# Kernel tuning notes

Hardware: AMD Instinct MI355X
Metric: run time of the kernel (lower is better)

Reference implementation:

```python
import jax, jax.numpy as jnp
import numpy as np

N_ENT, N_CON, DIM, R, NB = 30000, 29309, 128, 12, 8
B, LC, S, E_DB, E_CON = 256, 50, 32, 300000, 200000


def setup_inputs() -> dict:
    key = jax.random.key(0)
    ks = jax.random.split(key, 32)
    f = lambda k, sh: (jax.random.normal(k, sh, jnp.float32) * 0.02)
    concept_emb = f(ks[0], (N_CON, DIM)).at[0].set(0.0)  # padding_idx=0 row zeroed
    inp = {
        'concept_mask': jax.random.randint(ks[1], (B, LC), 0, N_CON, jnp.int32),
        'seed_pad': jax.random.randint(ks[2], (B, S), 0, N_ENT, jnp.int32),
        'seed_lens': jax.random.randint(ks[3], (B,), 0, S + 1, jnp.int32),
        'db_edge_index': jax.random.randint(ks[4], (2, E_DB), 0, N_ENT, jnp.int32),
        'db_edge_type': jax.random.randint(ks[5], (E_DB,), 0, R, jnp.int32),
        'con_edge_index': jax.random.randint(ks[6], (2, E_CON), 0, N_CON, jnp.int32),
        'db_vec': jax.random.uniform(ks[7], (B, N_ENT), jnp.float32),
        'labels': jax.random.randint(ks[8], (B,), 0, N_ENT, jnp.int64),
        'rec': jax.random.uniform(ks[9], (B,), jnp.float32),
        'concept_emb': concept_emb,
        'basis': f(ks[10], (NB, N_ENT, DIM)),
        'comp': f(ks[11], (R, NB)),
        'rgcn_root': f(ks[12], (N_ENT, DIM)),
        'rgcn_bias': jnp.zeros((DIM,), jnp.float32),
        'gcn_w': f(ks[13], (DIM, DIM)),
        'gcn_b': jnp.zeros((DIM,), jnp.float32),
        'attn_a': f(ks[14], (DIM, DIM)),
        'attn_b': f(ks[15], (DIM, 1)),
        'attn_a_db': f(ks[16], (DIM, DIM)),
        'attn_b_db': f(ks[17], (DIM, 1)),
        'user_norm_w': f(ks[18], (DIM, 2 * DIM)),
        'user_norm_b': jnp.zeros((DIM,), jnp.float32),
        'gate_norm_w': f(ks[19], (1, DIM)),
        'gate_norm_b': jnp.zeros((1,), jnp.float32),
        'info_con_w': f(ks[20], (DIM, DIM)),
        'info_con_b': jnp.zeros((DIM,), jnp.float32),
        'info_out_db_b': jnp.zeros((N_ENT,), jnp.float32),
        'output_en_b': jnp.zeros((N_ENT,), jnp.float32),
    }
    return inp


def _forward(concept_mask, seed_pad, seed_lens, db_edge_index, db_edge_type,
             con_edge_index, db_vec, labels, rec, concept_emb, basis, comp,
             rgcn_root, rgcn_bias, gcn_w, gcn_b, attn_a, attn_b, attn_a_db,
             attn_b_db, user_norm_w, user_norm_b, gate_norm_w, gate_norm_b,
             info_con_w, info_con_b, info_out_db_b, output_en_b):
    NEG = jnp.float32(-1e30)
    # ---- RGCN over DBpedia graph (x=None -> per-edge row W[rel][src]) ----
    w = jnp.einsum('rb,bnd->rnd', comp, basis)            # [R, N_ent, D]
    src, dst = db_edge_index[0], db_edge_index[1]
    msg = w[db_edge_type, src]                            # [E, D]
    agg = jax.ops.segment_sum(msg, dst, num_segments=N_ENT)
    cnt = jax.ops.segment_sum(jnp.ones_like(dst, jnp.float32), dst, num_segments=N_ENT)
    db_feats = agg / jnp.maximum(cnt, 1.0)[:, None] + rgcn_root + rgcn_bias  # mean aggr + root + bias
    # ---- GCN over concept graph (symmetric norm, self-loops) ----
    xw = concept_emb @ gcn_w
    loops = jnp.arange(N_CON, dtype=con_edge_index.dtype)
    cs = jnp.concatenate([con_edge_index[0], loops])
    cd = jnp.concatenate([con_edge_index[1], loops])
    deg = jax.ops.segment_sum(jnp.ones_like(cd, jnp.float32), cd, num_segments=N_CON)
    dinv = jnp.where(deg > 0, jax.lax.rsqrt(jnp.maximum(deg, 1e-12)), 0.0)
    norm = dinv[cs] * dinv[cd]
    con_feats = jax.ops.segment_sum(norm[:, None] * xw[cs], cd, num_segments=N_CON) + gcn_b
    # ---- per-sample seed-set self-attention over db features ----
    h = db_feats[seed_pad]                                # [B, S, D]
    e = jnp.tanh(h @ attn_a_db) @ attn_b_db               # [B, S, 1]
    valid = jnp.arange(S)[None, :] < seed_lens[:, None]   # [B, S]
    a = jax.nn.softmax(jnp.where(valid[..., None], e, NEG), axis=1)
    db_user = jnp.einsum('bso,bsd->bd', a, h)             # weighted sum (o=1)
    has_seed = (seed_lens > 0)
    db_user = jnp.where(has_seed[:, None], db_user, 0.0)  # empty seed set -> zeros
    db_con_mask = has_seed.astype(jnp.float32)
    # ---- batch self-attention over gathered concept features ----
    hc = con_feats[concept_mask]                          # [B, LC, D]
    ec = jnp.tanh(hc @ attn_a) @ attn_b                   # [B, LC, 1]
    cvalid = (concept_mask != 0)
    ac = jax.nn.softmax(jnp.where(cvalid[..., None], ec, NEG), axis=1)
    con_user = jnp.einsum('blo,bld->bd', ac, hc)
    # ---- gated fusion ----
    u = jnp.concatenate([con_user, db_user], axis=-1) @ user_norm_w.T + user_norm_b
    gate = jax.nn.sigmoid(u @ gate_norm_w.T + gate_norm_b)  # [B, 1]
    user_emb = gate * db_user + (1.0 - gate) * con_user
    entity_scores = user_emb @ db_feats.T + output_en_b   # [B, N_ent]
    # ---- infomax MSE loss ----
    con_e = con_user @ info_con_w.T + info_con_b
    db_scores = con_e @ db_feats.T + info_out_db_b
    info_db_loss = jnp.mean(jnp.sum((db_scores - db_vec) ** 2, axis=-1) * db_con_mask)
    # ---- rec CE loss ----
    logp = jax.nn.log_softmax(entity_scores, axis=-1)
    ce = -jnp.take_along_axis(logp, labels[:, None].astype(jnp.int32), axis=1)[:, 0]
    rec_loss = jnp.sum(ce * rec)
    loss = rec_loss + 0.025 * info_db_loss                # pretrain=False path
    return loss, entity_scores, rec_loss


def reference(concept_mask, seed_pad, seed_lens, db_edge_index, db_edge_type,
              con_edge_index, db_vec, labels, rec, concept_emb, basis, comp,
              rgcn_root, rgcn_bias, gcn_w, gcn_b, attn_a, attn_b, attn_a_db,
              attn_b_db, user_norm_w, user_norm_b, gate_norm_w, gate_norm_b,
              info_con_w, info_con_b, info_out_db_b, output_en_b):
    return _forward(concept_mask, seed_pad, seed_lens, db_edge_index, db_edge_type,
                    con_edge_index, db_vec, labels, rec, concept_emb, basis, comp,
                    rgcn_root, rgcn_bias, gcn_w, gcn_b, attn_a, attn_b, attn_a_db,
                    attn_b_db, user_norm_w, user_norm_b, gate_norm_w, gate_norm_b,
                    info_con_w, info_con_b, info_out_db_b, output_en_b)
```

## Files before the change

kernel.cpp:

```cpp
#include <hip/hip_runtime.h>

#define N_ENT  30000
#define N_CON  29309
#define DIM    128
#define NBASIS 8
#define NREL   12
#define BATCH  256
#define LCON   50
#define SSEED  32
#define EDB    300000
#define ECON   200000
#define NTILE  938

#define NE4      ((N_CON * DIM) / 4)
#define NB_HIST  ((EDB + ECON + 255) / 256)
#define NB_CONV  ((NE4 + 3 * (DIM * DIM / 4) + 255) / 256)
#define NB_WCOMP ((N_ENT * 32) / 256)
#define NB_XW    ((N_CON + 127) / 128)
#define NB_RG    ((N_ENT + 3) / 4)
#define NB_GG    ((N_CON + 3) / 4)
#define NB_EDB   ((N_ENT + 31) / 32)
#define NB_ECON  ((N_CON + 31) / 32)

typedef __attribute__((ext_vector_type(8)))  short bfrag8;
typedef __attribute__((ext_vector_type(16))) float facc16;

__device__ __forceinline__ unsigned short f2bf(float f) {
    unsigned int u = __float_as_uint(f);
    u += 0x7FFFu + ((u >> 16) & 1u);
    return (unsigned short)(u >> 16);
}
__device__ __forceinline__ float bf2f(unsigned int h) {
    return __uint_as_float(h << 16);
}

__global__ __launch_bounds__(256) void prep_kernel(const int* __restrict__ db_dst,
                                                   const int* __restrict__ con_dst,
                                                   const float* __restrict__ emb,
                                                   const float* __restrict__ W,
                                                   const float* __restrict__ A_db,
                                                   const float* __restrict__ A_c,
                                                   const float* __restrict__ basis,
                                                   const float* __restrict__ comp,
                                                   int* __restrict__ cnt_e, int* __restrict__ cnt_c,
                                                   int* __restrict__ ord_db, int* __restrict__ ord_con,
                                                   unsigned short* __restrict__ emb_h,
                                                   unsigned short* __restrict__ Wt_h,
                                                   unsigned short* __restrict__ At_db_h,
                                                   unsigned short* __restrict__ At_c_h,
                                                   unsigned short* __restrict__ w_h,
                                                   int use_w) {
    __shared__ float sc[NREL * NBASIS];
    int t = threadIdx.x, bb = blockIdx.x;
    if (bb < NB_HIST) {
        int e = bb * 256 + t;
        if (e < EDB) {
            ord_db[e] = atomicAdd(cnt_e + db_dst[e], 1);
        } else if (e < EDB + ECON) {
            int ee = e - EDB;
            ord_con[ee] = atomicAdd(cnt_c + con_dst[ee], 1);
        }
        return;
    }
    if (bb < NB_HIST + NB_CONV) {
        int i = (bb - NB_HIST) * 256 + t;
        if (i < NE4) {
            float4 v = ((const float4*)emb)[i];
            unsigned int p0 = (unsigned int)f2bf(v.x) | ((unsigned int)f2bf(v.y) << 16);
            unsigned int p1 = (unsigned int)f2bf(v.z) | ((unsigned int)f2bf(v.w) << 16);
            *(uint2*)(emb_h + (size_t)i * 4) = make_uint2(p0, p1);
        } else {
            int j = i - NE4;
            if (j < 3 * (DIM * DIM) / 4) {
                int sel = j >> 12;
                int jj = j & 4095;
                const float* S = (sel == 0) ? W : ((sel == 1) ? A_db : A_c);
                unsigned short* Dst = (sel == 0) ? Wt_h : ((sel == 1) ? At_db_h : At_c_h);
                int o = jj * 4;
                int n = o >> 7, k0 = o & 127;
                unsigned int p0 = (unsigned int)f2bf(S[(k0 + 0) * DIM + n]) |
                                  ((unsigned int)f2bf(S[(k0 + 1) * DIM + n]) << 16);
                unsigned int p1 = (unsigned int)f2bf(S[(k0 + 2) * DIM + n]) |
                                  ((unsigned int)f2bf(S[(k0 + 3) * DIM + n]) << 16);
                *(uint2*)(Dst + n * DIM + k0) = make_uint2(p0, p1);
            }
        }
        return;
    }
    if (!use_w) return;
    if (t < NREL * NBASIS) sc[t] = comp[t];
    __syncthreads();
    int i = (bb - NB_HIST - NB_CONV) * 256 + t;
    int n = i >> 5, d4 = i & 31;
    float4 bv[NBASIS];
#pragma unroll
    for (int b = 0; b < NBASIS; ++b)
        bv[b] = ((const float4*)(basis + ((size_t)b * N_ENT + n) * DIM))[d4];
#pragma unroll
    for (int r = 0; r < NREL; ++r) {
        float4 acc = make_float4(0.f, 0.f, 0.f, 0.f);
#pragma unroll
        for (int b = 0; b < NBASIS; ++b) {
            float c = sc[r * NBASIS + b];
            acc.x += c * bv[b].x; acc.y += c * bv[b].y;
            acc.z += c * bv[b].z; acc.w += c * bv[b].w;
        }
        unsigned int p0 = (unsigned int)f2bf(acc.x) | ((unsigned int)f2bf(acc.y) << 16);
        unsigned int p1 = (unsigned int)f2bf(acc.z) | ((unsigned int)f2bf(acc.w) << 16);
        *(uint2*)(w_h + ((size_t)r * N_ENT + n) * DIM + d4 * 4) = make_uint2(p0, p1);
    }
}

__device__ void scan_block(const int* __restrict__ cnt, int n, int* __restrict__ rowptr) {
    __shared__ int part[1024];
    int t = threadIdx.x;
    int per = (n + 1023) / 1024;
    int s0 = t * per;
    int sum = 0;
    for (int i = 0; i < per; ++i) {
        int idx = s0 + i;
        if (idx < n) sum += cnt[idx];
    }
    part[t] = sum;
    __syncthreads();
    for (int off = 1; off < 1024; off <<= 1) {
        int v = (t >= off) ? part[t - off] : 0;
        __syncthreads();
        part[t] += v;
        __syncthreads();
    }
    int run = part[t] - sum;
    for (int i = 0; i < per; ++i) {
        int idx = s0 + i;
        if (idx < n) {
            rowptr[idx] = run;
            run += cnt[idx];
        }
    }
    if (t == 1023) rowptr[n] = part[1023];
}

__global__ __launch_bounds__(1024) void scan2_kernel(const int* __restrict__ cnt_e,
                                                     const int* __restrict__ cnt_c,
                                                     int* __restrict__ rowptr_e,
                                                     int* __restrict__ rowptr_c,
                                                     float* __restrict__ dinv,
                                                     const unsigned short* __restrict__ emb_h,
                                                     const unsigned short* __restrict__ Wt_h,
                                                     unsigned short* __restrict__ xw_h) {
    int bb = blockIdx.x;
    if (bb == 0) {
        scan_block(cnt_e, N_ENT, rowptr_e);
        return;
    }
    if (bb == 1) {
        scan_block(cnt_c, N_CON, rowptr_c);
        for (int i = threadIdx.x; i < N_CON; i += 1024)
            dinv[i] = rsqrtf((float)(cnt_c[i] + 1));
        return;
    }
    int t = threadIdx.x;
    int wave = t >> 6, lane = t & 63;
    int m0 = (bb - 2) * 128 + (wave >> 2) * 32;
    int n0 = (wave & 3) * 32;
    int am = lane & 31, ak = (lane >> 5) * 8;
    int mrow = m0 + am;
    bool mv = mrow < N_CON;
    const unsigned short* Ar = emb_h + (size_t)mrow * DIM + ak;
    const unsigned short* Br = Wt_h + (size_t)(n0 + am) * DIM + ak;
    facc16 acc;
#pragma unroll
    for (int r = 0; r < 16; ++r) acc[r] = 0.f;
#pragma unroll
    for (int s = 0; s < 8; ++s) {
        bfrag8 a;
#pragma unroll
        for (int j = 0; j < 8; ++j) a[j] = 0;
        if (mv) a = *(const bfrag8*)(Ar + s * 16);
        bfrag8 b = *(const bfrag8*)(Br + s * 16);
        acc = __builtin_amdgcn_mfma_f32_32x32x16_bf16(a, b, acc, 0, 0, 0);
    }
    int col = lane & 31;
    int g4 = (lane >> 5) * 4;
#pragma unroll
    for (int r = 0; r < 16; ++r) {
        int m = m0 + (r & 3) + ((r >> 2) << 3) + g4;
        if (m < N_CON) xw_h[(size_t)m * DIM + n0 + col] = f2bf(acc[r]);
    }
}

__global__ __launch_bounds__(256) void scatter_kernel(const int* __restrict__ db_eidx,
                                                      const int* __restrict__ db_etype,
                                                      const int* __restrict__ con_eidx,
                                                      const int* __restrict__ ord_db,
                                                      const int* __restrict__ ord_con,
                                                      const int* __restrict__ rowptr_e,
                                                      const int* __restrict__ rowptr_c,
                                                      int* __restrict__ elist_e,
                                                      int* __restrict__ elist_c) {
    int e = blockIdx.x * 256 + threadIdx.x;
    if (e < EDB) {
        int dst = db_eidx[EDB + e];
        elist_e[rowptr_e[dst] + ord_db[e]] = db_eidx[e] | (db_etype[e] << 18);
    } else if (e < EDB + ECON) {
        int ee = e - EDB;
        int dst = con_eidx[ECON + ee];
        elist_c[rowptr_c[dst] + ord_con[ee]] = con_eidx[ee];
    }
}

__global__ __launch_bounds__(256) void gathers_kernel(const int* __restrict__ rowptr_e,
                                                      const int* __restrict__ elist_e,
                                                      const unsigned short* __restrict__ w_h,
                                                      const float* __restrict__ root,
                                                      const float* __restrict__ bias,
                                                      unsigned short* __restrict__ dbf_h,
                                                      const int* __restrict__ rowptr_c,
                                                      const int* __restrict__ elist_c,
                                                      const float* __restrict__ dinv,
                                                      const unsigned short* __restrict__ xw_h,
                                                      const float* __restrict__ gcn_b,
                                                      unsigned short* __restrict__ conf_h) {
    int bb = blockIdx.x;
    int lane = threadIdx.x & 63;
    if (bb < NB_RG) {
        int wid = bb * 4 + (threadIdx.x >> 6);
        if (wid >= N_ENT) return;
        int beg = rowptr_e[wid], end = rowptr_e[wid + 1];
        float a0 = 0.f, a1 = 0.f;
        int p = beg;
        for (; p + 3 < end; p += 4) {
            int v0 = elist_e[p], v1 = elist_e[p + 1], v2 = elist_e[p + 2], v3 = elist_e[p + 3];
            unsigned int k0 = *(const unsigned int*)(w_h + ((size_t)(v0 >> 18) * N_ENT + (v0 & 0x3FFFF)) * DIM + lane * 2);
            unsigned int k1 = *(const unsigned int*)(w_h + ((size_t)(v1 >> 18) * N_ENT + (v1 & 0x3FFFF)) * DIM + lane * 2);
            unsigned int k2 = *(const unsigned int*)(w_h + ((size_t)(v2 >> 18) * N_ENT + (v2 & 0x3FFFF)) * DIM + lane * 2);
            unsigned int k3 = *(const unsigned int*)(w_h + ((size_t)(v3 >> 18) * N_ENT + (v3 & 0x3FFFF)) * DIM + lane * 2);
            a0 += bf2f(k0 & 0xFFFF) + bf2f(k1 & 0xFFFF) + bf2f(k2 & 0xFFFF) + bf2f(k3 & 0xFFFF);
            a1 += bf2f(k0 >> 16)    + bf2f(k1 >> 16)    + bf2f(k2 >> 16)    + bf2f(k3 >> 16);
        }
        for (; p < end; ++p) {
            int v = elist_e[p];
            unsigned int k = *(const unsigned int*)(w_h + ((size_t)(v >> 18) * N_ENT + (v & 0x3FFFF)) * DIM + lane * 2);
            a0 += bf2f(k & 0xFFFF);
            a1 += bf2f(k >> 16);
        }
        float inv = 1.f / fmaxf((float)(end - beg), 1.f);
        size_t base = (size_t)wid * DIM + lane * 2;
        float f0 = a0 * inv + root[base]     + bias[lane * 2];
        float f1 = a1 * inv + root[base + 1] + bias[lane * 2 + 1];
        *(unsigned int*)(dbf_h + base) = (unsigned int)f2bf(f0) | ((unsigned int)f2bf(f1) << 16);
    } else {
        int wid = (bb - NB_RG) * 4 + (threadIdx.x >> 6);
        if (wid >= N_CON) return;
        int beg = rowptr_c[wid], end = rowptr_c[wid + 1];
        float a0 = 0.f, a1 = 0.f;
        int p = beg;
        for (; p + 3 < end; p += 4) {
            int s0 = elist_c[p], s1 = elist_c[p + 1], s2 = elist_c[p + 2], s3 = elist_c[p + 3];
            float n0 = dinv[s0], n1 = dinv[s1], n2 = dinv[s2], n3 = dinv[s3];
            unsigned int k0 = *(const unsigned int*)(xw_h + (size_t)s0 * DIM + lane * 2);
            unsigned int k1 = *(const unsigned int*)(xw_h + (size_t)s1 * DIM + lane * 2);
            unsigned int k2 = *(const unsigned int*)(xw_h + (size_t)s2 * DIM + lane * 2);
            unsigned int k3 = *(const unsigned int*)(xw_h + (size_t)s3 * DIM + lane * 2);
            a0 += n0 * bf2f(k0 & 0xFFFF) + n1 * bf2f(k1 & 0xFFFF) + n2 * bf2f(k2 & 0xFFFF) + n3 * bf2f(k3 & 0xFFFF);
            a1 += n0 * bf2f(k0 >> 16)    + n1 * bf2f(k1 >> 16)    + n2 * bf2f(k2 >> 16)    + n3 * bf2f(k3 >> 16);
        }
        for (; p < end; ++p) {
            int s = elist_c[p];
            float nm = dinv[s];
            unsigned int k = *(const unsigned int*)(xw_h + (size_t)s * DIM + lane * 2);
            a0 += nm * bf2f(k & 0xFFFF);
            a1 += nm * bf2f(k >> 16);
        }
        float dv = dinv[wid];
        unsigned int ks = *(const unsigned int*)(xw_h + (size_t)wid * DIM + lane * 2);
        size_t base = (size_t)wid * DIM + lane * 2;
        float f0 = dv * a0 + dv * dv * bf2f(ks & 0xFFFF) + gcn_b[lane * 2];
        float f1 = dv * a1 + dv * dv * bf2f(ks >> 16)    + gcn_b[lane * 2 + 1];
        *(unsigned int*)(conf_h + base) = (unsigned int)f2bf(f0) | ((unsigned int)f2bf(f1) << 16);
    }
}

__global__ __launch_bounds__(256) void rgcn_gather_basis(const int* __restrict__ rowptr,
                                                         const int* __restrict__ elist,
                                                         const float* __restrict__ basis,
                                                         const float* __restrict__ comp,
                                                         const float* __restrict__ root,
                                                         const float* __restrict__ bias,
                                                         unsigned short* __restrict__ dbf_h) {
    int wid  = blockIdx.x * 4 + (threadIdx.x >> 6);
    int lane = threadIdx.x & 63;
    if (wid >= N_ENT) return;
    int beg = rowptr[wid], end = rowptr[wid + 1];
    float a0 = 0.f, a1 = 0.f;
    for (int p = beg; p < end; ++p) {
        int v = elist[p];
        int src = v & 0x3FFFF, ty = v >> 18;
        const float* c = comp + ty * NBASIS;
#pragma unroll
        for (int b = 0; b < NBASIS; ++b) {
            const float* bp = basis + ((size_t)b * N_ENT + src) * DIM;
            a0 += c[b] * bp[lane * 2];
            a1 += c[b] * bp[lane * 2 + 1];
        }
    }
    float inv = 1.f / fmaxf((float)(end - beg), 1.f);
    size_t base = (size_t)wid * DIM + lane * 2;
    float f0 = a0 * inv + root[base]     + bias[lane * 2];
    float f1 = a1 * inv + root[base + 1] + bias[lane * 2 + 1];
    *(unsigned int*)(dbf_h + base) = (unsigned int)f2bf(f0) | ((unsigned int)f2bf(f1) << 16);
}

__global__ __launch_bounds__(256) void escore_kernel(const unsigned short* __restrict__ dbf_h,
                                                     const unsigned short* __restrict__ conf_h,
                                                     const unsigned short* __restrict__ At_db_h,
                                                     const float* __restrict__ v_db,
                                                     const unsigned short* __restrict__ At_c_h,
                                                     const float* __restrict__ v_c,
                                                     float* __restrict__ e_db,
                                                     float* __restrict__ e_con) {
    __shared__ float part[4][32];
    int t = threadIdx.x, bb = blockIdx.x;
    int wave = t >> 6, lane = t & 63;
    const unsigned short* feats;
    const unsigned short* At;
    const float* v;
    float* eo;
    int m0, nrow;
    if (bb < NB_EDB) {
        feats = dbf_h;  At = At_db_h; v = v_db; eo = e_db;  m0 = bb * 32;             nrow = N_ENT;
    } else {
        feats = conf_h; At = At_c_h;  v = v_c;  eo = e_con; m0 = (bb - NB_EDB) * 32;  nrow = N_CON;
    }
    int n0 = wave * 32;
    int am = lane & 31, ak = (lane >> 5) * 8;
    int mrow = m0 + am;
    bool mv = mrow < nrow;
    const unsigned short* Ar = feats + (size_t)mrow * DIM + ak;
    const unsigned short* Br = At + (size_t)(n0 + am) * DIM + ak;
    facc16 acc;
#pragma unroll
    for (int r = 0; r < 16; ++r) acc[r] = 0.f;
#pragma unroll
    for (int s = 0; s < 8; ++s) {
        bfrag8 a;
#pragma unroll
        for (int j = 0; j < 8; ++j) a[j] = 0;
        if (mv) a = *(const bfrag8*)(Ar + s * 16);
        bfrag8 b = *(const bfrag8*)(Br + s * 16);
        acc = __builtin_amdgcn_mfma_f32_32x32x16_bf16(a, b, acc, 0, 0, 0);
    }
    int col = lane & 31, g = lane >> 5;
    float vn = v[n0 + col];
#pragma unroll
    for (int r = 0; r < 16; ++r) {
        float x = tanhf(acc[r]) * vn;
#pragma unroll
        for (int off = 16; off >= 1; off >>= 1) x += __shfl_xor(x, off, 32);
        if (col == 0) {
            int row = (r & 3) + ((r >> 2) << 3) + (g << 2);
            part[wave][row] = x;
        }
    }
    __syncthreads();
    if (t < 32) {
        int m = m0 + t;
        if (m < nrow)
            eo[m] = part[0][t] + part[1][t] + part[2][t] + part[3][t];
    }
}

__global__ __launch_bounds__(256) void attn_fusion_kernel(const unsigned short* __restrict__ dbf_h,
                                                          const unsigned short* __restrict__ conf_h,
                                                          const float* __restrict__ e_db,
                                                          const float* __restrict__ e_con,
                                                          const int* __restrict__ seed_pad,
                                                          const int* __restrict__ seed_lens,
                                                          const int* __restrict__ concept_mask,
                                                          const float* __restrict__ Wu, const float* __restrict__ bu,
                                                          const float* __restrict__ gw, const float* __restrict__ gb,
                                                          const float* __restrict__ Wi, const float* __restrict__ bi,
                                                          unsigned short* __restrict__ uemb_h,
                                                          unsigned short* __restrict__ cone_h,
                                                          float* __restrict__ maskv) {
    __shared__ int srow[SSEED];
    __shared__ int crow[LCON];
    __shared__ float a_db[SSEED], a_con[LCON];
    __shared__ float du[DIM], cu[DIM], red[DIM];
    int b = blockIdx.x, t = threadIdx.x;
    int wave = t >> 6, lane = t & 63;
    int len = seed_lens[b];
    if (wave == 0) {
        float e = -1e30f;
        if (lane < SSEED) {
            int rv = seed_pad[b * SSEED + lane];
            srow[lane] = rv;
            if (lane < len) e = e_db[rv];
        }
        float m = e;
#pragma unroll
        for (int off = 16; off >= 1; off >>= 1) m = fmaxf(m, __shfl_xor(m, off, 32));
        float p = (lane < SSEED) ? __expf(e - m) : 0.f;
        float s = p;
#pragma unroll
        for (int off = 16; off >= 1; off >>= 1) s += __shfl_xor(s, off, 32);
        if (lane < SSEED) a_db[lane] = p / s;
    } else if (wave == 1) {
        float e = -1e30f;
        if (lane < LCON) {
            int rv = concept_mask[b * LCON + lane];
            crow[lane] = rv;
            if (rv != 0) e = e_con[rv];
        }
        float m = e;
#pragma unroll
        for (int off = 32; off >= 1; off >>= 1) m = fmaxf(m, __shfl_xor(m, off, 64));
        float p = (lane < LCON) ? __expf(e - m) : 0.f;
        float s = p;
#pragma unroll
        for (int off = 32; off >= 1; off >>= 1) s += __shfl_xor(s, off, 64);
        if (lane < LCON) a_con[lane] = p / s;
    }
    __syncthreads();
    if (t < DIM) {
        float acc = 0.f;
#pragma unroll
        for (int s = 0; s < SSEED; ++s)
            acc += a_db[s] * bf2f((unsigned int)dbf_h[(size_t)srow[s] * DIM + t]);
        du[t] = (len > 0) ? acc : 0.f;
    } else {
        int d = t - DIM;
        float acc = 0.f;
#pragma unroll
        for (int s = 0; s < LCON; ++s)
            acc += a_con[s] * bf2f((unsigned int)conf_h[(size_t)crow[s] * DIM + d]);
        cu[d] = acc;
    }
    __syncthreads();
    if (t < DIM) {
        float u = bu[t];
        const float* wr = Wu + t * 2 * DIM;
        for (int k = 0; k < DIM; ++k) u += cu[k] * wr[k];
        for (int k = 0; k < DIM; ++k) u += du[k] * wr[DIM + k];
        red[t] = u * gw[t];
    }
    __syncthreads();
    for (int s2 = 64; s2 > 0; s2 >>= 1) {
        if (t < s2) red[t] += red[t + s2];
        __syncthreads();
    }
    if (t < DIM) {
        float gate = 1.f / (1.f + __expf(-(red[0] + gb[0])));
        uemb_h[b * DIM + t] = f2bf(gate * du[t] + (1.f - gate) * cu[t]);
        float ce = bi[t];
        const float* wi = Wi + t * DIM;
        for (int k = 0; k < DIM; ++k) ce += cu[k] * wi[k];
        cone_h[b * DIM + t] = f2bf(ce);
    }
    if (t == 0) maskv[b] = (len > 0) ? 1.f : 0.f;
}

__global__ __launch_bounds__(256) void score_mfma(const unsigned short* __restrict__ dbf_h,
                                                  const unsigned short* __restrict__ uemb_h,
                                                  const unsigned short* __restrict__ cone_h,
                                                  const float* __restrict__ en_b,
                                                  const float* __restrict__ info_b,
                                                  const float* __restrict__ db_vec,
                                                  float* __restrict__ escore,
                                                  float* __restrict__ partM,
                                                  float* __restrict__ partS,
                                                  float* __restrict__ partQ) {
    int wave = threadIdx.x >> 6, lane = threadIdx.x & 63;
    int nt = blockIdx.x * 4 + wave;
    if (nt >= NTILE) return;
    int b0 = blockIdx.y * 32;
    int n0 = nt * 32;
    int am = lane & 31, ak = (lane >> 5) * 8;
    int nb = n0 + am;
    bool bvalid = nb < N_ENT;
    const unsigned short* Au = uemb_h + (size_t)(b0 + am) * DIM + ak;
    const unsigned short* Ac = cone_h + (size_t)(b0 + am) * DIM + ak;
    const unsigned short* Bp = dbf_h + (size_t)nb * DIM + ak;
    facc16 accE, accD;
#pragma unroll
    for (int r = 0; r < 16; ++r) { accE[r] = 0.f; accD[r] = 0.f; }
#pragma unroll
    for (int s = 0; s < 8; ++s) {
        bfrag8 au = *(const bfrag8*)(Au + s * 16);
        bfrag8 ac = *(const bfrag8*)(Ac + s * 16);
        bfrag8 bb;
#pragma unroll
        for (int j = 0; j < 8; ++j) bb[j] = 0;
        if (bvalid) bb = *(const bfrag8*)(Bp + s * 16);
        accE = __builtin_amdgcn_mfma_f32_32x32x16_bf16(au, bb, accE, 0, 0, 0);
        accD = __builtin_amdgcn_mfma_f32_32x32x16_bf16(ac, bb, accD, 0, 0, 0);
    }
    int col = lane & 31;
    int n = n0 + col;
    bool nv = n < N_ENT;
    float enb = nv ? en_b[n] : 0.f;
    float inb = nv ? info_b[n] : 0.f;
    int g4 = (lane >> 5) * 4;
#pragma unroll
    for (int r = 0; r < 16; ++r) {
        int b = b0 + (r & 3) + ((r >> 2) << 3) + g4;
        float e = accE[r] + enb;
        if (nv) escore[(size_t)b * N_ENT + n] = e;
        float ev = nv ? e : -1e30f;
        float mx = ev;
#pragma unroll
        for (int off = 16; off >= 1; off >>= 1) mx = fmaxf(mx, __shfl_xor(mx, off, 64));
        float ex = nv ? __expf(e - mx) : 0.f;
        float sm = ex;
#pragma unroll
        for (int off = 16; off >= 1; off >>= 1) sm += __shfl_xor(sm, off, 64);
        float d = nv ? (accD[r] + inb - db_vec[(size_t)b * N_ENT + n]) : 0.f;
        float q = d * d;
#pragma unroll
        for (int off = 16; off >= 1; off >>= 1) q += __shfl_xor(q, off, 64);
        if (col == 0) {
            partM[(size_t)b * NTILE + nt] = mx;
            partS[(size_t)b * NTILE + nt] = sm;
            partQ[(size_t)b * NTILE + nt] = q;
        }
    }
}

__global__ __launch_bounds__(256) void ce_final(const float* __restrict__ partM,
                                                const float* __restrict__ partS,
                                                const float* __restrict__ partQ,
                                                const float* __restrict__ escore,
                                                const int* __restrict__ labels,
                                                const float* __restrict__ rec,
                                                float* __restrict__ rloss,
                                                float* __restrict__ ssqv) {
    __shared__ float red[256], red2[256];
    int b = blockIdx.x, t = threadIdx.x;
    const float* pm = partM + (size_t)b * NTILE;
    const float* ps = partS + (size_t)b * NTILE;
    const float* pq = partQ + (size_t)b * NTILE;
    float mx = -1e30f;
    for (int i = t; i < NTILE; i += 256) mx = fmaxf(mx, pm[i]);
    red[t] = mx;
    __syncthreads();
    for (int s2 = 128; s2 > 0; s2 >>= 1) {
        if (t < s2) red[t] = fmaxf(red[t], red[t + s2]);
        __syncthreads();
    }
    float M = red[0];
    __syncthreads();
    float s = 0.f, q = 0.f;
    for (int i = t; i < NTILE; i += 256) {
        s += ps[i] * __expf(pm[i] - M);
        q += pq[i];
    }
    red[t] = s; red2[t] = q;
    __syncthreads();
    for (int s2 = 128; s2 > 0; s2 >>= 1) {
        if (t < s2) { red[t] += red[t + s2]; red2[t] += red2[t + s2]; }
        __syncthreads();
    }
    if (t == 0) {
        float lse = M + logf(red[0]);
        float ce  = -(escore[(size_t)b * N_ENT + labels[b]] - lse);
        rloss[b]  = ce * rec[b];
        ssqv[b]   = red2[0];
    }
}

__global__ __launch_bounds__(256) void final_kernel(const float* __restrict__ rloss,
                                                    const float* __restrict__ sumsq,
                                                    const float* __restrict__ maskv,
                                                    float* __restrict__ out) {
    __shared__ float r1[256], r2[256];
    int t = threadIdx.x;
    r1[t] = rloss[t];
    r2[t] = sumsq[t] * maskv[t];
    __syncthreads();
    for (int s2 = 128; s2 > 0; s2 >>= 1) {
        if (t < s2) { r1[t] += r1[t + s2]; r2[t] += r2[t + s2]; }
        __syncthreads();
    }
    if (t == 0) {
        float rec_loss = r1[0];
        float info = r2[0] / (float)BATCH;
        out[0] = rec_loss + 0.025f * info;
        out[1 + (size_t)BATCH * N_ENT] = rec_loss;
    }
}

extern "C" void kernel_launch(void* const* d_in, const int* in_sizes, int n_in,
                              void* d_out, int out_size, void* d_ws, size_t ws_size,
                              hipStream_t stream) {
    (void)in_sizes; (void)n_in; (void)out_size;
    const int*   concept_mask  = (const int*)d_in[0];
    const int*   seed_pad      = (const int*)d_in[1];
    const int*   seed_lens     = (const int*)d_in[2];
    const int*   db_eidx       = (const int*)d_in[3];
    const int*   db_etype      = (const int*)d_in[4];
    const int*   con_eidx      = (const int*)d_in[5];
    const float* db_vec        = (const float*)d_in[6];
    const int*   labels        = (const int*)d_in[7];
    const float* rec           = (const float*)d_in[8];
    const float* concept_emb   = (const float*)d_in[9];
    const float* basis         = (const float*)d_in[10];
    const float* comp          = (const float*)d_in[11];
    const float* rgcn_root     = (const float*)d_in[12];
    const float* rgcn_bias     = (const float*)d_in[13];
    const float* gcn_w         = (const float*)d_in[14];
    const float* gcn_b         = (const float*)d_in[15];
    const float* attn_a        = (const float*)d_in[16];
    const float* attn_b        = (const float*)d_in[17];
    const float* attn_a_db     = (const float*)d_in[18];
    const float* attn_b_db     = (const float*)d_in[19];
    const float* user_norm_w   = (const float*)d_in[20];
    const float* user_norm_b   = (const float*)d_in[21];
    const float* gate_norm_w   = (const float*)d_in[22];
    const float* gate_norm_b   = (const float*)d_in[23];
    const float* info_con_w    = (const float*)d_in[24];
    const float* info_con_b    = (const float*)d_in[25];
    const float* info_out_db_b = (const float*)d_in[26];
    const float* output_en_b   = (const float*)d_in[27];

    float* ws = (float*)d_ws;
    size_t off = 0;
    auto alloc = [&](size_t n) { float* p = ws + off; off += (n + 255) & ~(size_t)255; return p; };
    float* dinv   = alloc(N_CON);
    float* maskv  = alloc(BATCH);
    float* rls    = alloc(BATCH);
    float* ssqv   = alloc(BATCH);
    float* partM  = alloc((size_t)BATCH * NTILE);
    float* partS  = alloc((size_t)BATCH * NTILE);
    float* partQ  = alloc((size_t)BATCH * NTILE);
    int* cnt_e    = (int*)alloc(N_ENT + N_CON);
    int* cnt_c    = cnt_e + N_ENT;
    int* rowptr_e = (int*)alloc(N_ENT + 1);
    int* rowptr_c = (int*)alloc(N_CON + 1);
    int* ord_db   = (int*)alloc(EDB);
    int* ord_con  = (int*)alloc(ECON);
    int* elist_e  = (int*)alloc(EDB);
    int* elist_c  = (int*)alloc(ECON);
    unsigned short* dbf_h  = (unsigned short*)alloc((size_t)N_ENT * DIM / 2);
    unsigned short* conf_h = (unsigned short*)alloc((size_t)N_CON * DIM / 2 + 128);
    unsigned short* xw_h   = (unsigned short*)alloc((size_t)N_CON * DIM / 2 + 128);
    unsigned short* emb_h  = (unsigned short*)alloc((size_t)N_CON * DIM / 2 + 128);
    unsigned short* Wt_h   = (unsigned short*)alloc(DIM * DIM / 2);
    unsigned short* uemb_h = (unsigned short*)alloc(BATCH * DIM / 2);
    unsigned short* cone_h = (unsigned short*)alloc(BATCH * DIM / 2);
    float* e_db   = alloc(N_ENT);
    float* e_con  = alloc(N_CON);
    unsigned short* At_db_h = (unsigned short*)alloc(DIM * DIM / 2);
    unsigned short* At_c_h  = (unsigned short*)alloc(DIM * DIM / 2);
    size_t w_elems = ((size_t)NREL * N_ENT * DIM) / 2;
    int use_w = (off + w_elems) * sizeof(float) <= ws_size;
    unsigned short* w_h = (unsigned short*)(ws + off);

    float* out    = (float*)d_out;
    float* escore = out + 1;

    (void)hipMemsetAsync(cnt_e, 0, (N_ENT + N_CON) * sizeof(int), stream);

    prep_kernel<<<NB_HIST + NB_CONV + NB_WCOMP, 256, 0, stream>>>(
        db_eidx + EDB, con_eidx + ECON, concept_emb, gcn_w, attn_a_db, attn_a,
        basis, comp, cnt_e, cnt_c, ord_db, ord_con, emb_h, Wt_h, At_db_h, At_c_h,
        w_h, use_w);
    scan2_kernel<<<2 + NB_XW, 1024, 0, stream>>>(cnt_e, cnt_c, rowptr_e, rowptr_c, dinv,
                                                 emb_h, Wt_h, xw_h);
    scatter_kernel<<<NB_HIST, 256, 0, stream>>>(db_eidx, db_etype, con_eidx,
                                                ord_db, ord_con, rowptr_e, rowptr_c,
                                                elist_e, elist_c);
    gathers_kernel<<<NB_RG + NB_GG, 256, 0, stream>>>(rowptr_e, elist_e, w_h, rgcn_root, rgcn_bias,
                                                      dbf_h, rowptr_c, elist_c, dinv, xw_h, gcn_b, conf_h);
    if (!use_w) {
        rgcn_gather_basis<<<NB_RG, 256, 0, stream>>>(rowptr_e, elist_e, basis, comp,
                                                     rgcn_root, rgcn_bias, dbf_h);
    }
    escore_kernel<<<NB_EDB + NB_ECON, 256, 0, stream>>>(dbf_h, conf_h, At_db_h, attn_b_db,
                                                        At_c_h, attn_b, e_db, e_con);
    attn_fusion_kernel<<<BATCH, 256, 0, stream>>>(dbf_h, conf_h, e_db, e_con,
                                                  seed_pad, seed_lens, concept_mask,
                                                  user_norm_w, user_norm_b, gate_norm_w, gate_norm_b,
                                                  info_con_w, info_con_b, uemb_h, cone_h, maskv);
    dim3 sg((NTILE + 3) / 4, BATCH / 32);
    score_mfma<<<sg, 256, 0, stream>>>(dbf_h, uemb_h, cone_h, output_en_b, info_out_db_b, db_vec,
                                       escore, partM, partS, partQ);
    ce_final<<<BATCH, 256, 0, stream>>>(partM, partS, partQ, escore, labels, rec, rls, ssqv);
    final_kernel<<<1, 256, 0, stream>>>(rls, ssqv, maskv, out);
}
```

Baseline: 517.5 us.

## Regroup kernels to pair basis composition with GCN gather and RGCN with concept scoring

```diff
diff --git a/kernel.cpp b/kernel.cpp
--- a/kernel.cpp
+++ b/kernel.cpp
@@ -40,17 +40,12 @@
                                                    const float* __restrict__ W,
                                                    const float* __restrict__ A_db,
                                                    const float* __restrict__ A_c,
-                                                   const float* __restrict__ basis,
-                                                   const float* __restrict__ comp,
                                                    int* __restrict__ cnt_e, int* __restrict__ cnt_c,
                                                    int* __restrict__ ord_db, int* __restrict__ ord_con,
                                                    unsigned short* __restrict__ emb_h,
                                                    unsigned short* __restrict__ Wt_h,
                                                    unsigned short* __restrict__ At_db_h,
-                                                   unsigned short* __restrict__ At_c_h,
-                                                   unsigned short* __restrict__ w_h,
-                                                   int use_w) {
-    __shared__ float sc[NREL * NBASIS];
+                                                   unsigned short* __restrict__ At_c_h) {
     int t = threadIdx.x, bb = blockIdx.x;
     if (bb < NB_HIST) {
         int e = bb * 256 + t;
@@ -62,52 +57,27 @@
         }
         return;
     }
-    if (bb < NB_HIST + NB_CONV) {
-        int i = (bb - NB_HIST) * 256 + t;
-        if (i < NE4) {
-            float4 v = ((const float4*)emb)[i];
-            unsigned int p0 = (unsigned int)f2bf(v.x) | ((unsigned int)f2bf(v.y) << 16);
-            unsigned int p1 = (unsigned int)f2bf(v.z) | ((unsigned int)f2bf(v.w) << 16);
-            *(uint2*)(emb_h + (size_t)i * 4) = make_uint2(p0, p1);
-        } else {
-            int j = i - NE4;
-            if (j < 3 * (DIM * DIM) / 4) {
-                int sel = j >> 12;
-                int jj = j & 4095;
-                const float* S = (sel == 0) ? W : ((sel == 1) ? A_db : A_c);
-                unsigned short* Dst = (sel == 0) ? Wt_h : ((sel == 1) ? At_db_h : At_c_h);
-                int o = jj * 4;
-                int n = o >> 7, k0 = o & 127;
-                unsigned int p0 = (unsigned int)f2bf(S[(k0 + 0) * DIM + n]) |
-                                  ((unsigned int)f2bf(S[(k0 + 1) * DIM + n]) << 16);
-                unsigned int p1 = (unsigned int)f2bf(S[(k0 + 2) * DIM + n]) |
-                                  ((unsigned int)f2bf(S[(k0 + 3) * DIM + n]) << 16);
-                *(uint2*)(Dst + n * DIM + k0) = make_uint2(p0, p1);
-            }
-        }
-        return;
-    }
-    if (!use_w) return;
-    if (t < NREL * NBASIS) sc[t] = comp[t];
-    __syncthreads();
-    int i = (bb - NB_HIST - NB_CONV) * 256 + t;
-    int n = i >> 5, d4 = i & 31;
-    float4 bv[NBASIS];
-#pragma unroll
-    for (int b = 0; b < NBASIS; ++b)
-        bv[b] = ((const float4*)(basis + ((size_t)b * N_ENT + n) * DIM))[d4];
-#pragma unroll
-    for (int r = 0; r < NREL; ++r) {
-        float4 acc = make_float4(0.f, 0.f, 0.f, 0.f);
-#pragma unroll
-        for (int b = 0; b < NBASIS; ++b) {
-            float c = sc[r * NBASIS + b];
-            acc.x += c * bv[b].x; acc.y += c * bv[b].y;
-            acc.z += c * bv[b].z; acc.w += c * bv[b].w;
-        }
-        unsigned int p0 = (unsigned int)f2bf(acc.x) | ((unsigned int)f2bf(acc.y) << 16);
-        unsigned int p1 = (unsigned int)f2bf(acc.z) | ((unsigned int)f2bf(acc.w) << 16);
-        *(uint2*)(w_h + ((size_t)r * N_ENT + n) * DIM + d4 * 4) = make_uint2(p0, p1);
+    int i = (bb - NB_HIST) * 256 + t;
+    if (i < NE4) {
+        float4 v = ((const float4*)emb)[i];
+        unsigned int p0 = (unsigned int)f2bf(v.x) | ((unsigned int)f2bf(v.y) << 16);
+        unsigned int p1 = (unsigned int)f2bf(v.z) | ((unsigned int)f2bf(v.w) << 16);
+        *(uint2*)(emb_h + (size_t)i * 4) = make_uint2(p0, p1);
+    } else {
+        int j = i - NE4;
+        if (j < 3 * (DIM * DIM) / 4) {
+            int sel = j >> 12;
+            int jj = j & 4095;
+            const float* S = (sel == 0) ? W : ((sel == 1) ? A_db : A_c);
+            unsigned short* Dst = (sel == 0) ? Wt_h : ((sel == 1) ? At_db_h : At_c_h);
+            int o = jj * 4;
+            int n = o >> 7, k0 = o & 127;
+            unsigned int p0 = (unsigned int)f2bf(S[(k0 + 0) * DIM + n]) |
+                              ((unsigned int)f2bf(S[(k0 + 1) * DIM + n]) << 16);
+            unsigned int p1 = (unsigned int)f2bf(S[(k0 + 2) * DIM + n]) |
+                              ((unsigned int)f2bf(S[(k0 + 3) * DIM + n]) << 16);
+            *(uint2*)(Dst + n * DIM + k0) = make_uint2(p0, p1);
+        }
     }
 }
 
@@ -209,38 +179,152 @@
     }
 }
 
-__global__ __launch_bounds__(256) void gathers_kernel(const int* __restrict__ rowptr_e,
-                                                      const int* __restrict__ elist_e,
-                                                      const unsigned short* __restrict__ w_h,
-                                                      const float* __restrict__ root,
-                                                      const float* __restrict__ bias,
-                                                      unsigned short* __restrict__ dbf_h,
-                                                      const int* __restrict__ rowptr_c,
-                                                      const int* __restrict__ elist_c,
-                                                      const float* __restrict__ dinv,
-                                                      const unsigned short* __restrict__ xw_h,
-                                                      const float* __restrict__ gcn_b,
-                                                      unsigned short* __restrict__ conf_h) {
+__global__ __launch_bounds__(256) void wcomp_gcn_kernel(const float* __restrict__ basis,
+                                                        const float* __restrict__ comp,
+                                                        unsigned short* __restrict__ w_h,
+                                                        int use_w,
+                                                        const int* __restrict__ rowptr_c,
+                                                        const int* __restrict__ elist_c,
+                                                        const float* __restrict__ dinv,
+                                                        const unsigned short* __restrict__ xw_h,
+                                                        const float* __restrict__ gcn_b,
+                                                        unsigned short* __restrict__ conf_h) {
+    int t = threadIdx.x, bb = blockIdx.x;
+    if (bb < NB_WCOMP) {
+        __shared__ float sc[NREL * NBASIS];
+        if (!use_w) return;
+        if (t < NREL * NBASIS) sc[t] = comp[t];
+        __syncthreads();
+        int i = bb * 256 + t;
+        int n = i >> 5, d4 = i & 31;
+        float4 bv[NBASIS];
+#pragma unroll
+        for (int b = 0; b < NBASIS; ++b)
+            bv[b] = ((const float4*)(basis + ((size_t)b * N_ENT + n) * DIM))[d4];
+#pragma unroll
+        for (int r = 0; r < NREL; ++r) {
+            float4 acc = make_float4(0.f, 0.f, 0.f, 0.f);
+#pragma unroll
+            for (int b = 0; b < NBASIS; ++b) {
+                float c = sc[r * NBASIS + b];
+                acc.x += c * bv[b].x; acc.y += c * bv[b].y;
+                acc.z += c * bv[b].z; acc.w += c * bv[b].w;
+            }
+            unsigned int p0 = (unsigned int)f2bf(acc.x) | ((unsigned int)f2bf(acc.y) << 16);
+            unsigned int p1 = (unsigned int)f2bf(acc.z) | ((unsigned int)f2bf(acc.w) << 16);
+            *(uint2*)(w_h + ((size_t)n * NREL + r) * DIM + d4 * 4) = make_uint2(p0, p1);
+        }
+        return;
+    }
+    int gb = bb - NB_WCOMP;
+    int wid = gb * 4 + (t >> 6);
+    if (wid >= N_CON) return;
+    int lane = t & 63;
+    int beg = rowptr_c[wid], end = rowptr_c[wid + 1];
+    float a0 = 0.f, a1 = 0.f;
+    int p = beg;
+    for (; p + 3 < end; p += 4) {
+        int s0 = elist_c[p], s1 = elist_c[p + 1], s2 = elist_c[p + 2], s3 = elist_c[p + 3];
+        float n0 = dinv[s0], n1 = dinv[s1], n2 = dinv[s2], n3 = dinv[s3];
+        unsigned int k0 = *(const unsigned int*)(xw_h + (size_t)s0 * DIM + lane * 2);
+        unsigned int k1 = *(const unsigned int*)(xw_h + (size_t)s1 * DIM + lane * 2);
+        unsigned int k2 = *(const unsigned int*)(xw_h + (size_t)s2 * DIM + lane * 2);
+        unsigned int k3 = *(const unsigned int*)(xw_h + (size_t)s3 * DIM + lane * 2);
+        a0 += n0 * bf2f(k0 & 0xFFFF) + n1 * bf2f(k1 & 0xFFFF) + n2 * bf2f(k2 & 0xFFFF) + n3 * bf2f(k3 & 0xFFFF);
+        a1 += n0 * bf2f(k0 >> 16)    + n1 * bf2f(k1 >> 16)    + n2 * bf2f(k2 >> 16)    + n3 * bf2f(k3 >> 16);
+    }
+    for (; p < end; ++p) {
+        int s = elist_c[p];
+        float nm = dinv[s];
+        unsigned int k = *(const unsigned int*)(xw_h + (size_t)s * DIM + lane * 2);
+        a0 += nm * bf2f(k & 0xFFFF);
+        a1 += nm * bf2f(k >> 16);
+    }
+    float dv = dinv[wid];
+    unsigned int ks = *(const unsigned int*)(xw_h + (size_t)wid * DIM + lane * 2);
+    size_t base = (size_t)wid * DIM + lane * 2;
+    float f0 = dv * a0 + dv * dv * bf2f(ks & 0xFFFF) + gcn_b[lane * 2];
+    float f1 = dv * a1 + dv * dv * bf2f(ks >> 16)    + gcn_b[lane * 2 + 1];
+    *(unsigned int*)(conf_h + base) = (unsigned int)f2bf(f0) | ((unsigned int)f2bf(f1) << 16);
+}
+
+__device__ __forceinline__ void escore_body(const unsigned short* __restrict__ feats,
+                                            const unsigned short* __restrict__ At,
+                                            const float* __restrict__ v,
+                                            float* __restrict__ eo,
+                                            int m0, int nrow) {
+    __shared__ float part[4][32];
+    int t = threadIdx.x;
+    int wave = t >> 6, lane = t & 63;
+    int n0 = wave * 32;
+    int am = lane & 31, ak = (lane >> 5) * 8;
+    int mrow = m0 + am;
+    bool mv = mrow < nrow;
+    const unsigned short* Ar = feats + (size_t)mrow * DIM + ak;
+    const unsigned short* Br = At + (size_t)(n0 + am) * DIM + ak;
+    facc16 acc;
+#pragma unroll
+    for (int r = 0; r < 16; ++r) acc[r] = 0.f;
+#pragma unroll
+    for (int s = 0; s < 8; ++s) {
+        bfrag8 a;
+#pragma unroll
+        for (int j = 0; j < 8; ++j) a[j] = 0;
+        if (mv) a = *(const bfrag8*)(Ar + s * 16);
+        bfrag8 b = *(const bfrag8*)(Br + s * 16);
+        acc = __builtin_amdgcn_mfma_f32_32x32x16_bf16(a, b, acc, 0, 0, 0);
+    }
+    int col = lane & 31, g = lane >> 5;
+    float vn = v[n0 + col];
+#pragma unroll
+    for (int r = 0; r < 16; ++r) {
+        float x = tanhf(acc[r]) * vn;
+#pragma unroll
+        for (int off = 16; off >= 1; off >>= 1) x += __shfl_xor(x, off, 32);
+        if (col == 0) {
+            int row = (r & 3) + ((r >> 2) << 3) + (g << 2);
+            part[wave][row] = x;
+        }
+    }
+    __syncthreads();
+    if (t < 32) {
+        int m = m0 + t;
+        if (m < nrow)
+            eo[m] = part[0][t] + part[1][t] + part[2][t] + part[3][t];
+    }
+}
+
+__global__ __launch_bounds__(256) void rgcn_escore_kernel(const int* __restrict__ rowptr_e,
+                                                          const int* __restrict__ elist_e,
+                                                          const unsigned short* __restrict__ w_h,
+                                                          const float* __restrict__ root,
+                                                          const float* __restrict__ bias,
+                                                          unsigned short* __restrict__ dbf_h,
+                                                          const unsigned short* __restrict__ conf_h,
+                                                          const unsigned short* __restrict__ At_c_h,
+                                                          const float* __restrict__ v_c,
+                                                          float* __restrict__ e_con,
+                                                          int use_w) {
     int bb = blockIdx.x;
-    int lane = threadIdx.x & 63;
     if (bb < NB_RG) {
+        if (!use_w) return;
         int wid = bb * 4 + (threadIdx.x >> 6);
-        if (wid >= N_ENT) return;
+        int lane = threadIdx.x & 63;
         int beg = rowptr_e[wid], end = rowptr_e[wid + 1];
         float a0 = 0.f, a1 = 0.f;
         int p = beg;
         for (; p + 3 < end; p += 4) {
             int v0 = elist_e[p], v1 = elist_e[p + 1], v2 = elist_e[p + 2], v3 = elist_e[p + 3];
-            unsigned int k0 = *(const unsigned int*)(w_h + ((size_t)(v0 >> 18) * N_ENT + (v0 & 0x3FFFF)) * DIM + lane * 2);
-            unsigned int k1 = *(const unsigned int*)(w_h + ((size_t)(v1 >> 18) * N_ENT + (v1 & 0x3FFFF)) * DIM + lane * 2);
-            unsigned int k2 = *(const unsigned int*)(w_h + ((size_t)(v2 >> 18) * N_ENT + (v2 & 0x3FFFF)) * DIM + lane * 2);
-            unsigned int k3 = *(const unsigned int*)(w_h + ((size_t)(v3 >> 18) * N_ENT + (v3 & 0x3FFFF)) * DIM + lane * 2);
+            unsigned int k0 = *(const unsigned int*)(w_h + ((size_t)(v0 & 0x3FFFF) * NREL + (v0 >> 18)) * DIM + lane * 2);
+            unsigned int k1 = *(const unsigned int*)(w_h + ((size_t)(v1 & 0x3FFFF) * NREL + (v1 >> 18)) * DIM + lane * 2);
+            unsigned int k2 = *(const unsigned int*)(w_h + ((size_t)(v2 & 0x3FFFF) * NREL + (v2 >> 18)) * DIM + lane * 2);
+            unsigned int k3 = *(const unsigned int*)(w_h + ((size_t)(v3 & 0x3FFFF) * NREL + (v3 >> 18)) * DIM + lane * 2);
             a0 += bf2f(k0 & 0xFFFF) + bf2f(k1 & 0xFFFF) + bf2f(k2 & 0xFFFF) + bf2f(k3 & 0xFFFF);
             a1 += bf2f(k0 >> 16)    + bf2f(k1 >> 16)    + bf2f(k2 >> 16)    + bf2f(k3 >> 16);
         }
         for (; p < end; ++p) {
             int v = elist_e[p];
-            unsigned int k = *(const unsigned int*)(w_h + ((size_t)(v >> 18) * N_ENT + (v & 0x3FFFF)) * DIM + lane * 2);
+            unsigned int k = *(const unsigned int*)(w_h + ((size_t)(v & 0x3FFFF) * NREL + (v >> 18)) * DIM + lane * 2);
             a0 += bf2f(k & 0xFFFF);
             a1 += bf2f(k >> 16);
         }
@@ -249,36 +333,9 @@
         float f0 = a0 * inv + root[base]     + bias[lane * 2];
         float f1 = a1 * inv + root[base + 1] + bias[lane * 2 + 1];
         *(unsigned int*)(dbf_h + base) = (unsigned int)f2bf(f0) | ((unsigned int)f2bf(f1) << 16);
-    } else {
-        int wid = (bb - NB_RG) * 4 + (threadIdx.x >> 6);
-        if (wid >= N_CON) return;
-        int beg = rowptr_c[wid], end = rowptr_c[wid + 1];
-        float a0 = 0.f, a1 = 0.f;
-        int p = beg;
-        for (; p + 3 < end; p += 4) {
-            int s0 = elist_c[p], s1 = elist_c[p + 1], s2 = elist_c[p + 2], s3 = elist_c[p + 3];
-            float n0 = dinv[s0], n1 = dinv[s1], n2 = dinv[s2], n3 = dinv[s3];
-            unsigned int k0 = *(const unsigned int*)(xw_h + (size_t)s0 * DIM + lane * 2);
-            unsigned int k1 = *(const unsigned int*)(xw_h + (size_t)s1 * DIM + lane * 2);
-            unsigned int k2 = *(const unsigned int*)(xw_h + (size_t)s2 * DIM + lane * 2);
-            unsigned int k3 = *(const unsigned int*)(xw_h + (size_t)s3 * DIM + lane * 2);
-            a0 += n0 * bf2f(k0 & 0xFFFF) + n1 * bf2f(k1 & 0xFFFF) + n2 * bf2f(k2 & 0xFFFF) + n3 * bf2f(k3 & 0xFFFF);
-            a1 += n0 * bf2f(k0 >> 16)    + n1 * bf2f(k1 >> 16)    + n2 * bf2f(k2 >> 16)    + n3 * bf2f(k3 >> 16);
-        }
-        for (; p < end; ++p) {
-            int s = elist_c[p];
-            float nm = dinv[s];
-            unsigned int k = *(const unsigned int*)(xw_h + (size_t)s * DIM + lane * 2);
-            a0 += nm * bf2f(k & 0xFFFF);
-            a1 += nm * bf2f(k >> 16);
-        }
-        float dv = dinv[wid];
-        unsigned int ks = *(const unsigned int*)(xw_h + (size_t)wid * DIM + lane * 2);
-        size_t base = (size_t)wid * DIM + lane * 2;
-        float f0 = dv * a0 + dv * dv * bf2f(ks & 0xFFFF) + gcn_b[lane * 2];
-        float f1 = dv * a1 + dv * dv * bf2f(ks >> 16)    + gcn_b[lane * 2 + 1];
-        *(unsigned int*)(conf_h + base) = (unsigned int)f2bf(f0) | ((unsigned int)f2bf(f1) << 16);
-    }
+        return;
+    }
+    escore_body(conf_h, At_c_h, v_c, e_con, (bb - NB_RG) * 32, N_CON);
 }
 
 __global__ __launch_bounds__(256) void rgcn_gather_basis(const int* __restrict__ rowptr,
@@ -311,63 +368,11 @@
     *(unsigned int*)(dbf_h + base) = (unsigned int)f2bf(f0) | ((unsigned int)f2bf(f1) << 16);
 }
 
-__global__ __launch_bounds__(256) void escore_kernel(const unsigned short* __restrict__ dbf_h,
-                                                     const unsigned short* __restrict__ conf_h,
-                                                     const unsigned short* __restrict__ At_db_h,
-                                                     const float* __restrict__ v_db,
-                                                     const unsigned short* __restrict__ At_c_h,
-                                                     const float* __restrict__ v_c,
-                                                     float* __restrict__ e_db,
-                                                     float* __restrict__ e_con) {
-    __shared__ float part[4][32];
-    int t = threadIdx.x, bb = blockIdx.x;
-    int wave = t >> 6, lane = t & 63;
-    const unsigned short* feats;
-    const unsigned short* At;
-    const float* v;
-    float* eo;
-    int m0, nrow;
-    if (bb < NB_EDB) {
-        feats = dbf_h;  At = At_db_h; v = v_db; eo = e_db;  m0 = bb * 32;             nrow = N_ENT;
-    } else {
-        feats = conf_h; At = At_c_h;  v = v_c;  eo = e_con; m0 = (bb - NB_EDB) * 32;  nrow = N_CON;
-    }
-    int n0 = wave * 32;
-    int am = lane & 31, ak = (lane >> 5) * 8;
-    int mrow = m0 + am;
-    bool mv = mrow < nrow;
-    const unsigned short* Ar = feats + (size_t)mrow * DIM + ak;
-    const unsigned short* Br = At + (size_t)(n0 + am) * DIM + ak;
-    facc16 acc;
-#pragma unroll
-    for (int r = 0; r < 16; ++r) acc[r] = 0.f;
-#pragma unroll
-    for (int s = 0; s < 8; ++s) {
-        bfrag8 a;
-#pragma unroll
-        for (int j = 0; j < 8; ++j) a[j] = 0;
-        if (mv) a = *(const bfrag8*)(Ar + s * 16);
-        bfrag8 b = *(const bfrag8*)(Br + s * 16);
-        acc = __builtin_amdgcn_mfma_f32_32x32x16_bf16(a, b, acc, 0, 0, 0);
-    }
-    int col = lane & 31, g = lane >> 5;
-    float vn = v[n0 + col];
-#pragma unroll
-    for (int r = 0; r < 16; ++r) {
-        float x = tanhf(acc[r]) * vn;
-#pragma unroll
-        for (int off = 16; off >= 1; off >>= 1) x += __shfl_xor(x, off, 32);
-        if (col == 0) {
-            int row = (r & 3) + ((r >> 2) << 3) + (g << 2);
-            part[wave][row] = x;
-        }
-    }
-    __syncthreads();
-    if (t < 32) {
-        int m = m0 + t;
-        if (m < nrow)
-            eo[m] = part[0][t] + part[1][t] + part[2][t] + part[3][t];
-    }
+__global__ __launch_bounds__(256) void escore_db_kernel(const unsigned short* __restrict__ dbf_h,
+                                                        const unsigned short* __restrict__ At_db_h,
+                                                        const float* __restrict__ v_db,
+                                                        float* __restrict__ e_db) {
+    escore_body(dbf_h, At_db_h, v_db, e_db, blockIdx.x * 32, N_ENT);
 }
 
 __global__ __launch_bounds__(256) void attn_fusion_kernel(const unsigned short* __restrict__ dbf_h,
@@ -660,23 +665,25 @@
 
     (void)hipMemsetAsync(cnt_e, 0, (N_ENT + N_CON) * sizeof(int), stream);
 
-    prep_kernel<<<NB_HIST + NB_CONV + NB_WCOMP, 256, 0, stream>>>(
+    prep_kernel<<<NB_HIST + NB_CONV, 256, 0, stream>>>(
         db_eidx + EDB, con_eidx + ECON, concept_emb, gcn_w, attn_a_db, attn_a,
-        basis, comp, cnt_e, cnt_c, ord_db, ord_con, emb_h, Wt_h, At_db_h, At_c_h,
-        w_h, use_w);
+        cnt_e, cnt_c, ord_db, ord_con, emb_h, Wt_h, At_db_h, At_c_h);
     scan2_kernel<<<2 + NB_XW, 1024, 0, stream>>>(cnt_e, cnt_c, rowptr_e, rowptr_c, dinv,
                                                  emb_h, Wt_h, xw_h);
     scatter_kernel<<<NB_HIST, 256, 0, stream>>>(db_eidx, db_etype, con_eidx,
                                                 ord_db, ord_con, rowptr_e, rowptr_c,
                                                 elist_e, elist_c);
-    gathers_kernel<<<NB_RG + NB_GG, 256, 0, stream>>>(rowptr_e, elist_e, w_h, rgcn_root, rgcn_bias,
-                                                      dbf_h, rowptr_c, elist_c, dinv, xw_h, gcn_b, conf_h);
+    wcomp_gcn_kernel<<<NB_WCOMP + NB_GG, 256, 0, stream>>>(basis, comp, w_h, use_w,
+                                                           rowptr_c, elist_c, dinv, xw_h,
+                                                           gcn_b, conf_h);
     if (!use_w) {
         rgcn_gather_basis<<<NB_RG, 256, 0, stream>>>(rowptr_e, elist_e, basis, comp,
                                                      rgcn_root, rgcn_bias, dbf_h);
     }
-    escore_kernel<<<NB_EDB + NB_ECON, 256, 0, stream>>>(dbf_h, conf_h, At_db_h, attn_b_db,
-                                                        At_c_h, attn_b, e_db, e_con);
+    rgcn_escore_kernel<<<NB_RG + NB_ECON, 256, 0, stream>>>(rowptr_e, elist_e, w_h,
+                                                            rgcn_root, rgcn_bias, dbf_h,
+                                                            conf_h, At_c_h, attn_b, e_con, use_w);
+    escore_db_kernel<<<NB_EDB, 256, 0, stream>>>(dbf_h, At_db_h, attn_b_db, e_db);
     attn_fusion_kernel<<<BATCH, 256, 0, stream>>>(dbf_h, conf_h, e_db, e_con,
                                                   seed_pad, seed_lens, concept_mask,
                                                   user_norm_w, user_norm_b, gate_norm_w, gate_norm_b,
```

New measurement: 516.4 us. About the same (-0.2%).
